# Kernel tuning notes

Hardware: AMD Instinct MI355X
Metric: run time of the kernel (lower is better)

Reference implementation:

```python
import jax, jax.numpy as jnp
import numpy as np
import math

E, K, CAPF = 8, 2, 1.25
D, DFF = 512, 2048


def setup_inputs() -> dict:
    key = jax.random.key(0)
    ks = jax.random.split(key, 5)
    s = lambda k, sh, sc: (jax.random.normal(k, sh, jnp.float32) * sc)
    return {
        "x": jax.random.normal(ks[0], (8, 4096, D), jnp.float32),
        "Wr": s(ks[1], (D, E), 1.0 / math.sqrt(D)),
        "br": jnp.zeros((E,), jnp.float32),
        "W1": s(ks[2], (E, D, DFF), 1.0 / math.sqrt(D)),
        "b1": jnp.zeros((E, DFF), jnp.float32),
        "W2": s(ks[3], (E, DFF, D), 1.0 / math.sqrt(DFF)),
        "b2": jnp.zeros((E, D), jnp.float32),
    }


def _moe(x, Wr, br, W1, b1, W2, b2):
    orig = x.shape
    d = orig[-1]
    xf = x.reshape(-1, d)                     # [N, d]
    N = xf.shape[0]
    # --- TopK router ---
    logits = xf @ Wr + br                      # [N, E]
    probs = jax.nn.softmax(logits, axis=-1)
    topk_p, topk_i = jax.lax.top_k(probs, K)   # [N, K]
    topk_w = topk_p / (jnp.sum(topk_p, axis=-1, keepdims=True) + 1e-9)
    # --- Capacity-based sparse dispatch ---
    cap = max(1, int(math.ceil(CAPF * float(N * K) / float(E))))
    flat_e = topk_i.reshape(-1)                # [N*K] expert id per slot
    flat_w = topk_w.reshape(-1)                # [N*K]
    tok = jnp.repeat(jnp.arange(N), K)         # [N*K] source token id
    one_hot = jax.nn.one_hot(flat_e, E, dtype=xf.dtype)          # [N*K, E]
    pos = (jnp.cumsum(one_hot, axis=0) - one_hot)[jnp.arange(N * K), flat_e]
    pos = pos.astype(jnp.int32)                # position within expert buffer
    keep = pos < cap                           # tokens beyond capacity dropped
    w_k = jnp.where(keep, flat_w, 0.0)
    sum_w = jnp.zeros((N,), xf.dtype).at[tok].add(w_k)           # kept weight per token
    w_norm = w_k / (sum_w[tok] + 1e-9)
    slot = flat_e * cap + pos                  # flat index into [E*cap]
    slot_safe = jnp.where(keep, slot, E * cap) # out-of-bounds -> dropped by scatter
    expert_in = (jnp.zeros((E * cap, d), xf.dtype)
                 .at[slot_safe].set(xf[tok], mode="drop")
                 .reshape(E, cap, d))
    # --- Grouped expert FFN (exact GELU like torch nn.GELU) ---
    h = jax.nn.gelu(jnp.einsum("ecd,edf->ecf", expert_in, W1) + b1[:, None, :],
                    approximate=False)
    expert_out = (jnp.einsum("ecf,efd->ecd", h, W2) + b2[:, None, :]).reshape(E * cap, d)
    # --- Combine: gather back and weighted scatter-add per token ---
    contrib = expert_out[jnp.where(keep, slot, 0)]               # dropped -> w_norm=0
    y = jnp.zeros((N, d), xf.dtype).at[tok].add(contrib * w_norm[:, None])
    return y.reshape(orig)


def reference(x, Wr, br, W1, b1, W2, b2):
    return _moe(x, Wr, br, W1, b1, W2, b2)
```

## Files before the change

kernel.cpp:

```cpp
#include <hip/hip_runtime.h>
#include <cstdint>
#include <cstddef>

#define E_EXP 8
#define TOPK 2
#define DMODEL 512
#define DFFDIM 2048

typedef __attribute__((ext_vector_type(8))) short short8;
typedef __attribute__((ext_vector_type(4))) float f32x4;

__device__ __forceinline__ unsigned short f2bf(float f) {
    unsigned int u = __float_as_uint(f);
    u += 0x7fffu + ((u >> 16) & 1u);
    return (unsigned short)(u >> 16);
}

__global__ __launch_bounds__(256) void transpose_kernel(
    const float* __restrict__ in, unsigned short* __restrict__ out, int R, int C)
{
    __shared__ float tile[32][33];
    const float* ie = in + (size_t)blockIdx.z * R * C;
    unsigned short* oe = out + (size_t)blockIdx.z * R * C;
    int x = blockIdx.x * 32 + threadIdx.x;
#pragma unroll
    for (int i = 0; i < 4; i++) {
        int ry = blockIdx.y * 32 + threadIdx.y + i * 8;
        tile[threadIdx.y + i * 8][threadIdx.x] = ie[(size_t)ry * C + x];
    }
    __syncthreads();
    int xo = blockIdx.y * 32 + threadIdx.x;
#pragma unroll
    for (int i = 0; i < 4; i++) {
        int co = blockIdx.x * 32 + threadIdx.y + i * 8;
        oe[(size_t)co * R + xo] = f2bf(tile[threadIdx.x][threadIdx.y + i * 8]);
    }
}

__global__ __launch_bounds__(256) void router_kernel(
    const float* __restrict__ x, const float* __restrict__ Wr,
    const float* __restrict__ br, int N,
    int* __restrict__ e0e1, float2* __restrict__ w01)
{
    int lane = threadIdx.x & 63, wave = threadIdx.x >> 6;
    int t = blockIdx.x * 4 + wave;
    if (t >= N) return;
    const float* xr = x + (size_t)t * DMODEL;
    float4 v0 = *(const float4*)(xr + lane * 4);
    float4 v1 = *(const float4*)(xr + 256 + lane * 4);
    float xv[8] = {v0.x, v0.y, v0.z, v0.w, v1.x, v1.y, v1.z, v1.w};
    const float* wr0 = Wr + (size_t)lane * 32;
    const float* wr1 = Wr + (size_t)(256 + lane * 4) * 8;
    double acc[8];
#pragma unroll
    for (int j = 0; j < 8; j++) acc[j] = 0.0;
#pragma unroll
    for (int c = 0; c < 4; c++) {
#pragma unroll
        for (int j = 0; j < 8; j++) {
            acc[j] += (double)xv[c] * (double)wr0[c * 8 + j];
            acc[j] += (double)xv[4 + c] * (double)wr1[c * 8 + j];
        }
    }
#pragma unroll
    for (int j = 0; j < 8; j++) {
        double s = acc[j];
#pragma unroll
        for (int o = 32; o > 0; o >>= 1) s += __shfl_xor(s, o, 64);
        acc[j] = s;
    }
    if (lane == 0) {
        float l[8], p[8];
        float mx = -1e30f;
        for (int j = 0; j < 8; j++) { l[j] = (float)acc[j] + br[j]; mx = fmaxf(mx, l[j]); }
        float Z = 0.f;
        for (int j = 0; j < 8; j++) { p[j] = expf(l[j] - mx); Z += p[j]; }
        for (int j = 0; j < 8; j++) p[j] /= Z;
        int e0 = 0;
        for (int j = 1; j < 8; j++) if (l[j] > l[e0]) e0 = j;
        int e1 = (e0 == 0) ? 1 : 0;
        for (int j = 0; j < 8; j++) if (j != e0 && l[j] > l[e1]) e1 = j;
        float den = p[e0] + p[e1] + 1e-9f;
        e0e1[t] = e0 | (e1 << 8);
        w01[t] = make_float2(p[e0] / den, p[e1] / den);
    }
}

__global__ __launch_bounds__(256) void hist_kernel(
    const int* __restrict__ e0e1, int NK, int* __restrict__ hist)
{
    __shared__ int cnt[8];
    int t = threadIdx.x;
    if (t < 8) cnt[t] = 0;
    __syncthreads();
    int s = blockIdx.x * 256 + t;
    if (s < NK) {
        int pk = e0e1[s >> 1];
        int e = (s & 1) ? ((pk >> 8) & 255) : (pk & 255);
        atomicAdd(&cnt[e], 1);
    }
    __syncthreads();
    if (t < 8) hist[blockIdx.x * 8 + t] = cnt[t];
}

__global__ __launch_bounds__(256) void scan_kernel(
    const int* __restrict__ hist, int NB, int cap,
    int* __restrict__ base, int* __restrict__ cnt_used)
{
    __shared__ int buf[256];
    int t = threadIdx.x;
    for (int e = 0; e < 8; e++) {
        int v = (t < NB) ? hist[t * 8 + e] : 0;
        int val = v;
        buf[t] = val;
        __syncthreads();
        for (int o = 1; o < 256; o <<= 1) {
            int add = (t >= o) ? buf[t - o] : 0;
            __syncthreads();
            val += add;
            buf[t] = val;
            __syncthreads();
        }
        if (t < NB) base[t * 8 + e] = val - v;
        if (t == 255) cnt_used[e] = min(val, cap);
        __syncthreads();
    }
}

__global__ __launch_bounds__(256) void pos_kernel(
    const int* __restrict__ e0e1, const float2* __restrict__ w01,
    const int* __restrict__ base, int NK, int cap,
    int* __restrict__ sidx, int* __restrict__ tok_of, float* __restrict__ wslot)
{
    __shared__ int waveCnt[4][8];
    __shared__ float kw[256];
    int t = threadIdx.x, lane = t & 63, wave = t >> 6;
    int s = blockIdx.x * 256 + t;
    bool valid = s < NK;
    int e = 8; float w = 0.f;
    if (valid) {
        int pk = e0e1[s >> 1];
        float2 ww = w01[s >> 1];
        if (s & 1) { e = (pk >> 8) & 255; w = ww.y; }
        else       { e = pk & 255;        w = ww.x; }
    }
    unsigned long long mymask = 0ull;
#pragma unroll
    for (int j = 0; j < 8; j++) {
        unsigned long long m = __ballot(e == j);
        if (lane == j) waveCnt[wave][j] = __popcll(m);
        if (e == j) mymask = m;
    }
    __syncthreads();
    int wrank = __popcll(mymask & ((1ull << lane) - 1ull));
    int prior = 0;
    for (int w2 = 0; w2 < wave; w2++) prior += waveCnt[w2][e & 7];
    int pos = base[blockIdx.x * 8 + (e & 7)] + prior + wrank;
    bool keep = valid && (pos < cap);
    kw[t] = keep ? w : 0.f;
    __syncthreads();
    float sum = kw[t] + kw[t ^ 1];
    float wn = keep ? (kw[t] / (sum + 1e-9f)) : 0.f;
    if (valid) {
        int si = keep ? (e * cap + pos) : -1;
        sidx[s] = si;
        if (keep) { tok_of[si] = s >> 1; wslot[si] = wn; }
    }
}

__global__ __launch_bounds__(256) void scatter_kernel(
    const float* __restrict__ x, const int* __restrict__ sidx,
    unsigned short* __restrict__ Xe, int NK)
{
    int lane = threadIdx.x & 63, wave = threadIdx.x >> 6;
    int s = blockIdx.x * 4 + wave;
    if (s >= NK) return;
    int si = sidx[s];
    if (si < 0) return;
    int tok = s >> 1;
    const float* xr = x + (size_t)tok * DMODEL + lane * 8;
    float4 a = *(const float4*)xr;
    float4 b = *(const float4*)(xr + 4);
    short8 v;
    v[0] = (short)f2bf(a.x); v[1] = (short)f2bf(a.y);
    v[2] = (short)f2bf(a.z); v[3] = (short)f2bf(a.w);
    v[4] = (short)f2bf(b.x); v[5] = (short)f2bf(b.y);
    v[6] = (short)f2bf(b.z); v[7] = (short)f2bf(b.w);
    *(short8*)(Xe + (size_t)si * DMODEL + lane * 8) = v;
}

template <int MODE>
__global__ __launch_bounds__(256, 3) void gemm_kernel(
    const unsigned short* __restrict__ A, int lda, size_t aStrE,
    const unsigned short* __restrict__ B, int ldb, size_t bStrE,
    const float* __restrict__ bias, int biasStrE,
    void* __restrict__ out, size_t cStrE, int ldc,
    const int* __restrict__ cnt, const int* __restrict__ tok_of,
    const float* __restrict__ wslot, int cap, int Kext)
{
    __shared__ unsigned short As[2][128 * 32];
    __shared__ unsigned short Bs[2][128 * 32];
    int e = blockIdx.z;
    int m0 = blockIdx.y * 128, n0 = blockIdx.x * 128;
    int M = cnt[e];
    if (m0 >= M) return;
    const unsigned short* Ae = A + (size_t)e * aStrE;
    const unsigned short* Be = B + (size_t)e * bStrE;

    int t = threadIdx.x, lane = t & 63, wave = t >> 6;
    int row = t >> 2, seg = (t & 3) * 8;
    const unsigned short* ga = Ae + (size_t)(m0 + row) * lda + seg;
    const unsigned short* gb = Be + (size_t)(n0 + row) * ldb + seg;
    unsigned short* la0 = &As[0][t * 8];
    unsigned short* la1 = &As[0][(t + 256) * 8];
    unsigned short* lb0 = &Bs[0][t * 8];
    unsigned short* lb1 = &Bs[0][(t + 256) * 8];

    f32x4 acc[4][4];
#pragma unroll
    for (int i = 0; i < 4; i++)
#pragma unroll
        for (int j = 0; j < 4; j++) acc[i][j] = (f32x4){0.f, 0.f, 0.f, 0.f};

    int wm = (wave & 1) * 64, wn = (wave >> 1) * 64;
    int lr = lane & 15, lq = lane >> 4;
    const unsigned short* pa = &As[0][(wm + lr) * 32 + lq * 8];
    const unsigned short* pb = &Bs[0][(wn + lr) * 32 + lq * 8];

    short8 ra0 = *(const short8*)ga;
    short8 ra1 = *(const short8*)(ga + (size_t)64 * lda);
    short8 rb0 = *(const short8*)gb;
    short8 rb1 = *(const short8*)(gb + (size_t)64 * ldb);
    ga += 32; gb += 32;
    *(short8*)la0 = ra0; *(short8*)la1 = ra1;
    *(short8*)lb0 = rb0; *(short8*)lb1 = rb1;
    __syncthreads();

    int buf = 0;
    for (int k0 = 32; k0 < Kext; k0 += 32) {
        ra0 = *(const short8*)ga;
        ra1 = *(const short8*)(ga + (size_t)64 * lda);
        rb0 = *(const short8*)gb;
        rb1 = *(const short8*)(gb + (size_t)64 * ldb);
        ga += 32; gb += 32;
        {
            int bo = buf * (128 * 32);
            short8 af[4], bf[4];
#pragma unroll
            for (int i = 0; i < 4; i++) af[i] = *(const short8*)(pa + bo + i * 16 * 32);
#pragma unroll
            for (int j = 0; j < 4; j++) bf[j] = *(const short8*)(pb + bo + j * 16 * 32);
#pragma unroll
            for (int i = 0; i < 4; i++)
#pragma unroll
                for (int j = 0; j < 4; j++)
                    acc[i][j] = __builtin_amdgcn_mfma_f32_16x16x32_bf16(af[i], bf[j], acc[i][j], 0, 0, 0);
        }
        int nbo = (buf ^ 1) * (128 * 32);
        *(short8*)(la0 + nbo) = ra0; *(short8*)(la1 + nbo) = ra1;
        *(short8*)(lb0 + nbo) = rb0; *(short8*)(lb1 + nbo) = rb1;
        __syncthreads();
        buf ^= 1;
    }
    {
        int bo = buf * (128 * 32);
        short8 af[4], bf[4];
#pragma unroll
        for (int i = 0; i < 4; i++) af[i] = *(const short8*)(pa + bo + i * 16 * 32);
#pragma unroll
        for (int j = 0; j < 4; j++) bf[j] = *(const short8*)(pb + bo + j * 16 * 32);
#pragma unroll
        for (int i = 0; i < 4; i++)
#pragma unroll
            for (int j = 0; j < 4; j++)
                acc[i][j] = __builtin_amdgcn_mfma_f32_16x16x32_bf16(af[i], bf[j], acc[i][j], 0, 0, 0);
    }

    if (MODE == 0) {
        size_t cb = (size_t)e * cStrE;
#pragma unroll
        for (int j = 0; j < 4; j++) {
            int n = n0 + wn + j * 16 + lr;
            float bv = bias[(size_t)e * biasStrE + n];
#pragma unroll
            for (int i = 0; i < 4; i++) {
                int mbase = m0 + wm + i * 16 + lq * 4;
                f32x4 v = acc[i][j];
#pragma unroll
                for (int r = 0; r < 4; r++) {
                    float val = v[r] + bv;
                    val = 0.5f * val * (1.0f + erff(val * 0.7071067811865475f));
                    ((unsigned short*)out)[cb + (size_t)(mbase + r) * ldc + n] = f2bf(val);
                }
            }
        }
    } else {
        float wv[4][4]; int tv[4][4];
#pragma unroll
        for (int i = 0; i < 4; i++) {
            int mbase = m0 + wm + i * 16 + lq * 4;
#pragma unroll
            for (int r = 0; r < 4; r++) {
                int m = mbase + r;
                if (m < M) { int sl = e * cap + m; wv[i][r] = wslot[sl]; tv[i][r] = tok_of[sl]; }
                else       { wv[i][r] = 0.f; tv[i][r] = -1; }
            }
        }
        float* y = (float*)out;
#pragma unroll
        for (int j = 0; j < 4; j++) {
            int n = n0 + wn + j * 16 + lr;
            float bv = bias[(size_t)e * biasStrE + n];
#pragma unroll
            for (int i = 0; i < 4; i++) {
                f32x4 v = acc[i][j];
#pragma unroll
                for (int r = 0; r < 4; r++) {
                    if (tv[i][r] >= 0)
                        atomicAdd(y + (size_t)tv[i][r] * ldc + n, wv[i][r] * (v[r] + bv));
                }
            }
        }
    }
}

extern "C" void kernel_launch(void* const* d_in, const int* in_sizes, int n_in,
                              void* d_out, int out_size, void* d_ws, size_t ws_size,
                              hipStream_t stream)
{
    const float* x  = (const float*)d_in[0];
    const float* Wr = (const float*)d_in[1];
    const float* br = (const float*)d_in[2];
    const float* W1 = (const float*)d_in[3];
    const float* b1 = (const float*)d_in[4];
    const float* W2 = (const float*)d_in[5];
    const float* b2 = (const float*)d_in[6];
    float* y = (float*)d_out;
    (void)n_in;

    const int N = in_sizes[0] / DMODEL;
    const int NK = N * TOPK;
    const int cap = (NK * 5 + 31) / 32;
    const int mTiles = (cap + 127) / 128;
    const int NB = (NK + 255) / 256;

    size_t fixed = (size_t)E_EXP * DMODEL * DFFDIM * 2 * 2
                 + (size_t)E_EXP * cap * DMODEL * 2
                 + (size_t)N * 12 + (size_t)NK * 4 + (size_t)E_EXP * cap * 8
                 + (size_t)NB * 64 + (1 << 16);
    int G = E_EXP;
    while (G > 1 && fixed + (size_t)G * cap * DFFDIM * 2 > ws_size) G >>= 1;
    const int nGroups = E_EXP / G;

    char* ws = (char*)d_ws;
    size_t off = 0;
    auto take = [&](size_t bytes) {
        char* p = ws + off;
        off = (off + bytes + 255) & ~(size_t)255;
        return p;
    };
    unsigned short* W1t = (unsigned short*)take((size_t)E_EXP * DMODEL * DFFDIM * 2);
    unsigned short* W2t = (unsigned short*)take((size_t)E_EXP * DMODEL * DFFDIM * 2);
    unsigned short* Xe  = (unsigned short*)take((size_t)E_EXP * cap * DMODEL * 2);
    unsigned short* Hg  = (unsigned short*)take((size_t)G * cap * DFFDIM * 2);
    int*    e0e1 = (int*)take((size_t)N * 4);
    float2* w01  = (float2*)take((size_t)N * 8);
    int*    hist = (int*)take((size_t)NB * 8 * 4);
    int*    base = (int*)take((size_t)NB * 8 * 4);
    int*    cnt  = (int*)take(64);
    int*    sidx = (int*)take((size_t)NK * 4);
    int*    tok_of = (int*)take((size_t)E_EXP * cap * 4);
    float*  wslot  = (float*)take((size_t)E_EXP * cap * 4);

    transpose_kernel<<<dim3(DFFDIM / 32, DMODEL / 32, E_EXP), dim3(32, 8), 0, stream>>>(W1, W1t, DMODEL, DFFDIM);
    transpose_kernel<<<dim3(DMODEL / 32, DFFDIM / 32, E_EXP), dim3(32, 8), 0, stream>>>(W2, W2t, DFFDIM, DMODEL);
    router_kernel<<<(N + 3) / 4, 256, 0, stream>>>(x, Wr, br, N, e0e1, w01);
    hist_kernel<<<NB, 256, 0, stream>>>(e0e1, NK, hist);
    scan_kernel<<<1, 256, 0, stream>>>(hist, NB, cap, base, cnt);
    pos_kernel<<<NB, 256, 0, stream>>>(e0e1, w01, base, NK, cap, sidx, tok_of, wslot);
    scatter_kernel<<<(NK + 3) / 4, 256, 0, stream>>>(x, sidx, Xe, NK);
    hipMemsetAsync(d_out, 0, (size_t)out_size * 4, stream);

    for (int g = 0; g < nGroups; g++) {
        int e0 = g * G;
        gemm_kernel<0><<<dim3(DFFDIM / 128, mTiles, G), 256, 0, stream>>>(
            Xe + (size_t)e0 * cap * DMODEL, DMODEL, (size_t)cap * DMODEL,
            W1t + (size_t)e0 * DFFDIM * DMODEL, DMODEL, (size_t)DFFDIM * DMODEL,
            b1 + (size_t)e0 * DFFDIM, DFFDIM,
            Hg, (size_t)cap * DFFDIM, DFFDIM,
            cnt + e0, tok_of, wslot, cap, DMODEL);
        gemm_kernel<1><<<dim3(DMODEL / 128, mTiles, G), 256, 0, stream>>>(
            Hg, DFFDIM, (size_t)cap * DFFDIM,
            W2t + (size_t)e0 * DMODEL * DFFDIM, DFFDIM, (size_t)DMODEL * DFFDIM,
            b2 + (size_t)e0 * DMODEL, DMODEL,
            y, 0, DMODEL,
            cnt + e0, tok_of + (size_t)e0 * cap, wslot + (size_t)e0 * cap, cap, DFFDIM);
    }
}
```

Measured before the change: 992.7 us.

## Use direct global-to-LDS loads, swizzled LDS, XCD-aware tile mapping and split-K

Replaces the register-staged global loads with global_load_lds direct-to-shared transfers, and XOR-swizzles the LDS layout to cut bank conflicts on MFMA fragment reads. Blocks are remapped into a 1D grid so consecutive block ids (round-robined across the 8 XCDs) share an expert and n-tile, with m-tiles interleaved across XCDs. The second GEMM gains split-K by 2 over the hidden dimension, adding the bias only in the first split and relying on the existing atomics. This doubles atomic traffic on the output in exchange for more parallelism.

```diff
diff --git a/kernel.cpp b/kernel.cpp
--- a/kernel.cpp
+++ b/kernel.cpp
@@ -14,6 +14,12 @@
     unsigned int u = __float_as_uint(f);
     u += 0x7fffu + ((u >> 16) & 1u);
     return (unsigned short)(u >> 16);
+}
+
+__device__ __forceinline__ void gll16(const void* g, void* l) {
+    __builtin_amdgcn_global_load_lds(
+        (const __attribute__((address_space(1))) unsigned int*)g,
+        (__attribute__((address_space(3))) unsigned int*)l, 16, 0, 0);
 }
 
 __global__ __launch_bounds__(256) void transpose_kernel(
@@ -196,25 +202,40 @@
     const float* __restrict__ bias, int biasStrE,
     void* __restrict__ out, size_t cStrE, int ldc,
     const int* __restrict__ cnt, const int* __restrict__ tok_of,
-    const float* __restrict__ wslot, int cap, int Kext)
-{
-    __shared__ unsigned short As[2][128 * 32];
-    __shared__ unsigned short Bs[2][128 * 32];
-    int e = blockIdx.z;
-    int m0 = blockIdx.y * 128, n0 = blockIdx.x * 128;
+    const float* __restrict__ wslot, int cap, int Kfull,
+    int nTiles, int kSplit, int mbT)
+{
+    __shared__ unsigned short As[2 * 128 * 32];
+    __shared__ unsigned short Bs[2 * 128 * 32];
+
+    int lin = blockIdx.x;
+    int r = lin & 7, q = lin >> 3;
+    int perE = mbT * nTiles * kSplit;
+    int e = q / perE, rem = q - e * perE;
+    int n0i = rem % nTiles;
+    int rem2 = rem / nTiles;
+    int ks = rem2 % kSplit;
+    int mloc = rem2 / kSplit;
+    int m0 = (r * mbT + mloc) * 128;
+    int n0 = n0i * 128;
+    int kLen = Kfull / kSplit;
+    int kBase = ks * kLen;
+    int kIters = kLen / 32;
+
     int M = cnt[e];
     if (m0 >= M) return;
     const unsigned short* Ae = A + (size_t)e * aStrE;
     const unsigned short* Be = B + (size_t)e * bStrE;
 
     int t = threadIdx.x, lane = t & 63, wave = t >> 6;
-    int row = t >> 2, seg = (t & 3) * 8;
-    const unsigned short* ga = Ae + (size_t)(m0 + row) * lda + seg;
-    const unsigned short* gb = Be + (size_t)(n0 + row) * ldb + seg;
-    unsigned short* la0 = &As[0][t * 8];
-    unsigned short* la1 = &As[0][(t + 256) * 8];
-    unsigned short* lb0 = &Bs[0][t * 8];
-    unsigned short* lb1 = &Bs[0][(t + 256) * 8];
+    int row = t >> 2;
+    int segp = ((t & 3) ^ ((row >> 1) & 3)) * 8;
+    const unsigned short* ga = Ae + (size_t)(m0 + row) * lda + kBase + segp;
+    const unsigned short* gb = Be + (size_t)(n0 + row) * ldb + kBase + segp;
+    unsigned short* la0 = As + t * 8;
+    unsigned short* la1 = As + (t + 256) * 8;
+    unsigned short* lb0 = Bs + t * 8;
+    unsigned short* lb1 = Bs + (t + 256) * 8;
 
     f32x4 acc[4][4];
 #pragma unroll
@@ -224,51 +245,47 @@
 
     int wm = (wave & 1) * 64, wn = (wave >> 1) * 64;
     int lr = lane & 15, lq = lane >> 4;
-    const unsigned short* pa = &As[0][(wm + lr) * 32 + lq * 8];
-    const unsigned short* pb = &Bs[0][(wn + lr) * 32 + lq * 8];
-
-    short8 ra0 = *(const short8*)ga;
-    short8 ra1 = *(const short8*)(ga + (size_t)64 * lda);
-    short8 rb0 = *(const short8*)gb;
-    short8 rb1 = *(const short8*)(gb + (size_t)64 * ldb);
+    int xr = (lr >> 1) & 3;
+    const unsigned short* pa = As + (wm + lr) * 32 + (lq ^ xr) * 8;
+    const unsigned short* pb = Bs + (wn + lr) * 32 + (lq ^ xr) * 8;
+
+    gll16(ga, la0);
+    gll16(ga + (size_t)64 * lda, la1);
+    gll16(gb, lb0);
+    gll16(gb + (size_t)64 * ldb, lb1);
     ga += 32; gb += 32;
-    *(short8*)la0 = ra0; *(short8*)la1 = ra1;
-    *(short8*)lb0 = rb0; *(short8*)lb1 = rb1;
     __syncthreads();
 
     int buf = 0;
-    for (int k0 = 32; k0 < Kext; k0 += 32) {
-        ra0 = *(const short8*)ga;
-        ra1 = *(const short8*)(ga + (size_t)64 * lda);
-        rb0 = *(const short8*)gb;
-        rb1 = *(const short8*)(gb + (size_t)64 * ldb);
+    for (int k = 1; k < kIters; k++) {
+        int nb = buf ^ 1;
+        int nbo = nb * 4096;
+        gll16(ga, la0 + nbo);
+        gll16(ga + (size_t)64 * lda, la1 + nbo);
+        gll16(gb, lb0 + nbo);
+        gll16(gb + (size_t)64 * ldb, lb1 + nbo);
         ga += 32; gb += 32;
-        {
-            int bo = buf * (128 * 32);
-            short8 af[4], bf[4];
-#pragma unroll
-            for (int i = 0; i < 4; i++) af[i] = *(const short8*)(pa + bo + i * 16 * 32);
-#pragma unroll
-            for (int j = 0; j < 4; j++) bf[j] = *(const short8*)(pb + bo + j * 16 * 32);
-#pragma unroll
-            for (int i = 0; i < 4; i++)
-#pragma unroll
-                for (int j = 0; j < 4; j++)
-                    acc[i][j] = __builtin_amdgcn_mfma_f32_16x16x32_bf16(af[i], bf[j], acc[i][j], 0, 0, 0);
-        }
-        int nbo = (buf ^ 1) * (128 * 32);
-        *(short8*)(la0 + nbo) = ra0; *(short8*)(la1 + nbo) = ra1;
-        *(short8*)(lb0 + nbo) = rb0; *(short8*)(lb1 + nbo) = rb1;
+        int bo = buf * 4096;
+        short8 af[4], bf[4];
+#pragma unroll
+        for (int i = 0; i < 4; i++) af[i] = *(const short8*)(pa + bo + i * 512);
+#pragma unroll
+        for (int j = 0; j < 4; j++) bf[j] = *(const short8*)(pb + bo + j * 512);
+#pragma unroll
+        for (int i = 0; i < 4; i++)
+#pragma unroll
+            for (int j = 0; j < 4; j++)
+                acc[i][j] = __builtin_amdgcn_mfma_f32_16x16x32_bf16(af[i], bf[j], acc[i][j], 0, 0, 0);
         __syncthreads();
-        buf ^= 1;
+        buf = nb;
     }
     {
-        int bo = buf * (128 * 32);
+        int bo = buf * 4096;
         short8 af[4], bf[4];
 #pragma unroll
-        for (int i = 0; i < 4; i++) af[i] = *(const short8*)(pa + bo + i * 16 * 32);
-#pragma unroll
-        for (int j = 0; j < 4; j++) bf[j] = *(const short8*)(pb + bo + j * 16 * 32);
+        for (int i = 0; i < 4; i++) af[i] = *(const short8*)(pa + bo + i * 512);
+#pragma unroll
+        for (int j = 0; j < 4; j++) bf[j] = *(const short8*)(pb + bo + j * 512);
 #pragma unroll
         for (int i = 0; i < 4; i++)
 #pragma unroll
@@ -287,10 +304,10 @@
                 int mbase = m0 + wm + i * 16 + lq * 4;
                 f32x4 v = acc[i][j];
 #pragma unroll
-                for (int r = 0; r < 4; r++) {
-                    float val = v[r] + bv;
+                for (int rr = 0; rr < 4; rr++) {
+                    float val = v[rr] + bv;
                     val = 0.5f * val * (1.0f + erff(val * 0.7071067811865475f));
-                    ((unsigned short*)out)[cb + (size_t)(mbase + r) * ldc + n] = f2bf(val);
+                    ((unsigned short*)out)[cb + (size_t)(mbase + rr) * ldc + n] = f2bf(val);
                 }
             }
         }
@@ -300,24 +317,24 @@
         for (int i = 0; i < 4; i++) {
             int mbase = m0 + wm + i * 16 + lq * 4;
 #pragma unroll
-            for (int r = 0; r < 4; r++) {
-                int m = mbase + r;
-                if (m < M) { int sl = e * cap + m; wv[i][r] = wslot[sl]; tv[i][r] = tok_of[sl]; }
-                else       { wv[i][r] = 0.f; tv[i][r] = -1; }
+            for (int rr = 0; rr < 4; rr++) {
+                int m = mbase + rr;
+                if (m < M) { int sl = e * cap + m; wv[i][rr] = wslot[sl]; tv[i][rr] = tok_of[sl]; }
+                else       { wv[i][rr] = 0.f; tv[i][rr] = -1; }
             }
         }
         float* y = (float*)out;
 #pragma unroll
         for (int j = 0; j < 4; j++) {
             int n = n0 + wn + j * 16 + lr;
-            float bv = bias[(size_t)e * biasStrE + n];
+            float bv = (ks == 0) ? bias[(size_t)e * biasStrE + n] : 0.f;
 #pragma unroll
             for (int i = 0; i < 4; i++) {
                 f32x4 v = acc[i][j];
 #pragma unroll
-                for (int r = 0; r < 4; r++) {
-                    if (tv[i][r] >= 0)
-                        atomicAdd(y + (size_t)tv[i][r] * ldc + n, wv[i][r] * (v[r] + bv));
+                for (int rr = 0; rr < 4; rr++) {
+                    if (tv[i][rr] >= 0)
+                        atomicAdd(y + (size_t)tv[i][rr] * ldc + n, wv[i][rr] * (v[rr] + bv));
                 }
             }
         }
@@ -342,6 +359,7 @@
     const int NK = N * TOPK;
     const int cap = (NK * 5 + 31) / 32;
     const int mTiles = (cap + 127) / 128;
+    const int mbT = (mTiles + 7) / 8;
     const int NB = (NK + 255) / 256;
 
     size_t fixed = (size_t)E_EXP * DMODEL * DFFDIM * 2 * 2
@@ -381,19 +399,21 @@
     scatter_kernel<<<(NK + 3) / 4, 256, 0, stream>>>(x, sidx, Xe, NK);
     hipMemsetAsync(d_out, 0, (size_t)out_size * 4, stream);
 
+    const int nT1 = DFFDIM / 128, kS1 = 1;
+    const int nT2 = DMODEL / 128, kS2 = 2;
     for (int g = 0; g < nGroups; g++) {
         int e0 = g * G;
-        gemm_kernel<0><<<dim3(DFFDIM / 128, mTiles, G), 256, 0, stream>>>(
+        gemm_kernel<0><<<G * 8 * mbT * nT1 * kS1, 256, 0, stream>>>(
             Xe + (size_t)e0 * cap * DMODEL, DMODEL, (size_t)cap * DMODEL,
             W1t + (size_t)e0 * DFFDIM * DMODEL, DMODEL, (size_t)DFFDIM * DMODEL,
             b1 + (size_t)e0 * DFFDIM, DFFDIM,
             Hg, (size_t)cap * DFFDIM, DFFDIM,
-            cnt + e0, tok_of, wslot, cap, DMODEL);
-        gemm_kernel<1><<<dim3(DMODEL / 128, mTiles, G), 256, 0, stream>>>(
+            cnt + e0, tok_of, wslot, cap, DMODEL, nT1, kS1, mbT);
+        gemm_kernel<1><<<G * 8 * mbT * nT2 * kS2, 256, 0, stream>>>(
             Hg, DFFDIM, (size_t)cap * DFFDIM,
             W2t + (size_t)e0 * DMODEL * DFFDIM, DFFDIM, (size_t)DMODEL * DFFDIM,
             b2 + (size_t)e0 * DMODEL, DMODEL,
             y, 0, DMODEL,
-            cnt + e0, tok_of + (size_t)e0 * cap, wslot + (size_t)e0 * cap, cap, DFFDIM);
-    }
-}
+            cnt + e0, tok_of + (size_t)e0 * cap, wslot + (size_t)e0 * cap, cap, DFFDIM, nT2, kS2, mbT);
+    }
+}
```

New measurement: 1.106 ms. 11.4% more time.
